# Performance work log

Measured on AMD Instinct MI355X. Metric: run time of the kernel, lower is better.

The kernel has to match this reference:

```python
import jax, jax.numpy as jnp
import numpy as np

HIDDEN_DIM = 1024
BLOCK = 8
NUM_BLOCKS = HIDDEN_DIM // BLOCK


def setup_inputs() -> dict:
    key = jax.random.key(0)
    k1, k2, k3, k4 = jax.random.split(key, 4)
    B, S, D = 4, 4096, HIDDEN_DIM
    return {
        "x_real": jax.random.normal(k1, (B, S, D), dtype=jnp.float32),
        "x_imag": jax.random.normal(k2, (B, S, D), dtype=jnp.float32),
        "A_real": jax.random.normal(k3, (NUM_BLOCKS, BLOCK, BLOCK), dtype=jnp.float32) * 0.02,
        "A_imag": jax.random.normal(k4, (NUM_BLOCKS, BLOCK, BLOCK), dtype=jnp.float32) * 0.02,
    }


def _cayley_unitary(A_real, A_imag):
    # Enforce anti-Hermitian generator: A_r skew-symmetric, A_i symmetric.
    A_r = (A_real - jnp.swapaxes(A_real, -2, -1)) * 0.5
    A_i = (A_imag + jnp.swapaxes(A_imag, -2, -1)) * 0.5
    eye = jnp.eye(BLOCK, dtype=A_real.dtype)[None]  # [1, B, B]
    IpA_r = eye + A_r
    ImA_r = eye - A_r
    # Real-block isomorphism of complex system (I+A) U = (I-A)
    LHS = jnp.concatenate([
        jnp.concatenate([IpA_r, -A_i], axis=-1),
        jnp.concatenate([A_i, IpA_r], axis=-1),
    ], axis=-2)  # [N, 2B, 2B]
    RHS = jnp.concatenate([
        jnp.concatenate([ImA_r, A_i], axis=-1),
        jnp.concatenate([-A_i, ImA_r], axis=-1),
    ], axis=-2)  # [N, 2B, 2B]
    U_rb = jnp.linalg.solve(LHS, RHS)
    return U_rb[:, :BLOCK, :BLOCK], U_rb[:, BLOCK:, :BLOCK]  # (U_real, U_imag)


def reference(x_real, x_imag, A_real, A_imag):
    B, S, D = x_real.shape
    U_real, U_imag = _cayley_unitary(A_real, A_imag)  # each [N, Bk, Bk]
    xr = x_real.reshape(B, S, NUM_BLOCKS, BLOCK)
    xi = x_imag.reshape(B, S, NUM_BLOCKS, BLOCK)
    # Block-diagonal complex matmul: out = U @ x per block
    out_r = jnp.einsum('noi,bsni->bsno', U_real, xr) - jnp.einsum('noi,bsni->bsno', U_imag, xi)
    out_i = jnp.einsum('noi,bsni->bsno', U_real, xi) + jnp.einsum('noi,bsni->bsno', U_imag, xr)
    # Stack real/imag parts of the complex output: [2, B, S, D]
    return jnp.stack([out_r.reshape(B, S, D), out_i.reshape(B, S, D)])
```

## Files before the change

### kernel.cpp

```cpp
#include <hip/hip_runtime.h>

#define NBLK 128
#define BLK  8
#define BB   4
#define SS   4096
#define DD   1024
#define PLANE (BB * SS * DD)
#define APPLY_WGS 1024
#define THREADS (APPLY_WGS * 256)
#define NITER (PLANE / 4 / THREADS)

typedef float floatx4 __attribute__((ext_vector_type(4)));

__global__ __launch_bounds__(256) void cayley_kernel(
    const float* __restrict__ Ar, const float* __restrict__ Ai,
    float* __restrict__ Ur, float* __restrict__ Ui) {
  __shared__ float piv[16][33];
  const int s = threadIdx.x >> 4;
  const int r = threadIdx.x & 15;
  const int n = blockIdx.x * 16 + s;
  const float* arb = Ar + n * 64;
  const float* aib = Ai + n * 64;

  float row[32];
  if (r < 8) {
    #pragma unroll
    for (int c = 0; c < 8; ++c) {
      float sk = 0.5f * (arb[r * 8 + c] - arb[c * 8 + r]);
      float sy = 0.5f * (aib[r * 8 + c] + aib[c * 8 + r]);
      float d  = (c == r) ? 1.0f : 0.0f;
      row[c]      = d + sk;
      row[8 + c]  = -sy;
      row[16 + c] = d - sk;
      row[24 + c] = sy;
    }
  } else {
    const int rr = r - 8;
    #pragma unroll
    for (int c = 0; c < 8; ++c) {
      float sk = 0.5f * (arb[rr * 8 + c] - arb[c * 8 + rr]);
      float sy = 0.5f * (aib[rr * 8 + c] + aib[c * 8 + rr]);
      float d  = (c == rr) ? 1.0f : 0.0f;
      row[c]      = sy;
      row[8 + c]  = d + sk;
      row[16 + c] = -sy;
      row[24 + c] = d - sk;
    }
  }

  #pragma unroll
  for (int k = 0; k < 16; ++k) {
    if (r == k) {
      float inv = 1.0f / row[k];
      #pragma unroll
      for (int j = 0; j < 32; ++j) { row[j] *= inv; piv[s][j] = row[j]; }
    }
    __syncthreads();
    if (r != k) {
      float f = row[k];
      #pragma unroll
      for (int j = 0; j < 32; ++j) row[j] = fmaf(-f, piv[s][j], row[j]);
    }
    __syncthreads();
  }

  if (r < 8) {
    #pragma unroll
    for (int c = 0; c < 8; ++c) Ur[n * 64 + r * 8 + c] = row[16 + c];
  } else {
    #pragma unroll
    for (int c = 0; c < 8; ++c) Ui[n * 64 + (r - 8) * 8 + c] = row[16 + c];
  }
}

__global__ __launch_bounds__(256, 4) void apply_kernel(
    const float* __restrict__ xr, const float* __restrict__ xi,
    const float* __restrict__ Urg, const float* __restrict__ Uig,
    float* __restrict__ out) {
  const int G = blockIdx.x * 256 + threadIdx.x;
  const int p = G & 255;
  const int n = p >> 1;
  const int h = p & 1;

  float u[4][8], v[4][8];
  #pragma unroll
  for (int j = 0; j < 4; ++j) {
    const float* urow = Urg + n * 64 + (h * 4 + j) * 8;
    const float* vrow = Uig + n * 64 + (h * 4 + j) * 8;
    float4 uo = *(const float4*)(urow + h * 4);
    float4 up = *(const float4*)(urow + (h ^ 1) * 4);
    float4 vo = *(const float4*)(vrow + h * 4);
    float4 vp = *(const float4*)(vrow + (h ^ 1) * 4);
    u[j][0] = uo.x; u[j][1] = uo.y; u[j][2] = uo.z; u[j][3] = uo.w;
    u[j][4] = up.x; u[j][5] = up.y; u[j][6] = up.z; u[j][7] = up.w;
    v[j][0] = vo.x; v[j][1] = vo.y; v[j][2] = vo.z; v[j][3] = vo.w;
    v[j][4] = vp.x; v[j][5] = vp.y; v[j][6] = vp.z; v[j][7] = vp.w;
  }
  #pragma unroll
  for (int j = 0; j < 4; ++j)
    #pragma unroll
    for (int c = 0; c < 8; ++c)
      asm volatile("" : "+v"(u[j][c]), "+v"(v[j][c]));

  const float4* pxr = (const float4*)xr + G;
  const float4* pxi = (const float4*)xi + G;
  floatx4* qor = (floatx4*)out + G;
  floatx4* qoi = (floatx4*)(out + PLANE) + G;

  #pragma unroll 2
  for (int k = 0; k < NITER; ++k) {
    float4 a = *pxr;
    float4 b = *pxi;
    float oxr[4] = {a.x, a.y, a.z, a.w};
    float oxi[4] = {b.x, b.y, b.z, b.w};
    float pxr_[4], pxi_[4];
    #pragma unroll
    for (int c = 0; c < 4; ++c) {
      pxr_[c] = __shfl_xor(oxr[c], 1, 64);
      pxi_[c] = __shfl_xor(oxi[c], 1, 64);
    }

    floatx4 sr, si;
    #pragma unroll
    for (int j = 0; j < 4; ++j) {
      float r0 = u[j][0] * oxr[0];
      float i0 = u[j][0] * oxi[0];
      #pragma unroll
      for (int c = 1; c < 4; ++c) {
        r0 = fmaf(u[j][c], oxr[c], r0);
        i0 = fmaf(u[j][c], oxi[c], i0);
      }
      #pragma unroll
      for (int c = 0; c < 4; ++c) {
        r0 = fmaf(u[j][4 + c], pxr_[c], r0);
        i0 = fmaf(u[j][4 + c], pxi_[c], i0);
      }
      #pragma unroll
      for (int c = 0; c < 4; ++c) {
        r0 = fmaf(-v[j][c], oxi[c], r0);
        i0 = fmaf(v[j][c], oxr[c], i0);
      }
      #pragma unroll
      for (int c = 0; c < 4; ++c) {
        r0 = fmaf(-v[j][4 + c], pxi_[c], r0);
        i0 = fmaf(v[j][4 + c], pxr_[c], i0);
      }
      sr[j] = r0;
      si[j] = i0;
    }

    __builtin_nontemporal_store(sr, qor);
    __builtin_nontemporal_store(si, qoi);

    pxr += THREADS; pxi += THREADS; qor += THREADS; qoi += THREADS;
  }
}

extern "C" void kernel_launch(void* const* d_in, const int* in_sizes, int n_in,
                              void* d_out, int out_size, void* d_ws, size_t ws_size,
                              hipStream_t stream) {
  const float* xr = (const float*)d_in[0];
  const float* xi = (const float*)d_in[1];
  const float* Ar = (const float*)d_in[2];
  const float* Ai = (const float*)d_in[3];
  float* out = (float*)d_out;

  float* Ur = (float*)d_ws;
  float* Ui = Ur + NBLK * 64;

  cayley_kernel<<<8, 256, 0, stream>>>(Ar, Ai, Ur, Ui);
  apply_kernel<<<APPLY_WGS, 256, 0, stream>>>(xr, xi, Ur, Ui, out);
}
```

Baseline: 61.62 us.

## Load partner half-block from memory instead of cross-lane shuffles; shrink cayley workgroups

The apply kernel now loads the neighbouring lane's float4 directly from global memory (idx^1) instead of exchanging it with __shfl_xor, so the cross-lane DPP/LDS traffic goes away at the cost of twice as many load instructions. The second load should hit in L1/L2 because the adjacent lane requests the same line. The cayley solve kernel runs with 64-thread workgroups spread over 32 blocks instead of 256 threads over 8 blocks, which makes each __syncthreads cheaper and spreads the work over more CUs.

```diff
diff --git a/kernel.cpp b/kernel.cpp
--- a/kernel.cpp
+++ b/kernel.cpp
@@ -12,13 +12,13 @@
 
 typedef float floatx4 __attribute__((ext_vector_type(4)));
 
-__global__ __launch_bounds__(256) void cayley_kernel(
+__global__ __launch_bounds__(64) void cayley_kernel(
     const float* __restrict__ Ar, const float* __restrict__ Ai,
     float* __restrict__ Ur, float* __restrict__ Ui) {
-  __shared__ float piv[16][33];
+  __shared__ float piv[4][33];
   const int s = threadIdx.x >> 4;
   const int r = threadIdx.x & 15;
-  const int n = blockIdx.x * 16 + s;
+  const int n = blockIdx.x * 4 + s;
   const float* arb = Ar + n * 64;
   const float* aib = Ai + n * 64;
 
@@ -102,23 +102,23 @@
     for (int c = 0; c < 8; ++c)
       asm volatile("" : "+v"(u[j][c]), "+v"(v[j][c]));
 
-  const float4* pxr = (const float4*)xr + G;
-  const float4* pxi = (const float4*)xi + G;
-  floatx4* qor = (floatx4*)out + G;
-  floatx4* qoi = (floatx4*)(out + PLANE) + G;
+  const float4* pxr = (const float4*)xr;
+  const float4* pxi = (const float4*)xi;
+  floatx4* qor = (floatx4*)out;
+  floatx4* qoi = (floatx4*)(out + PLANE);
 
   #pragma unroll 2
   for (int k = 0; k < NITER; ++k) {
-    float4 a = *pxr;
-    float4 b = *pxi;
+    const int idx = k * THREADS + G;
+    float4 a  = pxr[idx];
+    float4 ap = pxr[idx ^ 1];
+    float4 b  = pxi[idx];
+    float4 bp = pxi[idx ^ 1];
+
     float oxr[4] = {a.x, a.y, a.z, a.w};
     float oxi[4] = {b.x, b.y, b.z, b.w};
-    float pxr_[4], pxi_[4];
-    #pragma unroll
-    for (int c = 0; c < 4; ++c) {
-      pxr_[c] = __shfl_xor(oxr[c], 1, 64);
-      pxi_[c] = __shfl_xor(oxi[c], 1, 64);
-    }
+    float wxr[4] = {ap.x, ap.y, ap.z, ap.w};
+    float wxi[4] = {bp.x, bp.y, bp.z, bp.w};
 
     floatx4 sr, si;
     #pragma unroll
@@ -132,8 +132,8 @@
       }
       #pragma unroll
       for (int c = 0; c < 4; ++c) {
-        r0 = fmaf(u[j][4 + c], pxr_[c], r0);
-        i0 = fmaf(u[j][4 + c], pxi_[c], i0);
+        r0 = fmaf(u[j][4 + c], wxr[c], r0);
+        i0 = fmaf(u[j][4 + c], wxi[c], i0);
       }
       #pragma unroll
       for (int c = 0; c < 4; ++c) {
@@ -142,17 +142,15 @@
       }
       #pragma unroll
       for (int c = 0; c < 4; ++c) {
-        r0 = fmaf(-v[j][4 + c], pxi_[c], r0);
-        i0 = fmaf(v[j][4 + c], pxr_[c], i0);
+        r0 = fmaf(-v[j][4 + c], wxi[c], r0);
+        i0 = fmaf(v[j][4 + c], wxr[c], i0);
       }
       sr[j] = r0;
       si[j] = i0;
     }
 
-    __builtin_nontemporal_store(sr, qor);
-    __builtin_nontemporal_store(si, qoi);
-
-    pxr += THREADS; pxi += THREADS; qor += THREADS; qoi += THREADS;
+    __builtin_nontemporal_store(sr, qor + idx);
+    __builtin_nontemporal_store(si, qoi + idx);
   }
 }
 
@@ -168,6 +166,6 @@
   float* Ur = (float*)d_ws;
   float* Ui = Ur + NBLK * 64;
 
-  cayley_kernel<<<8, 256, 0, stream>>>(Ar, Ai, Ur, Ui);
+  cayley_kernel<<<32, 64, 0, stream>>>(Ar, Ai, Ur, Ui);
   apply_kernel<<<APPLY_WGS, 256, 0, stream>>>(xr, xi, Ur, Ui, out);
 }
```

Measured after the change: 60.40 us. 2.0% less time.
